# Performance work log

Measured on AMD Instinct MI355X. Metric: run time of the kernel, lower is better.

## Reference

```python
import jax, jax.numpy as jnp
import numpy as np

N = 100000   # graph is [N, N]
NNZ = 1600000
D = 32

def setup_inputs() -> dict:
    key = jax.random.key(0)
    k1, k2, k3 = jax.random.split(key, 3)
    indices = jax.random.randint(k1, (2, NNZ), 0, N, dtype=jnp.int64)
    values = jax.random.uniform(k2, (NNZ,), dtype=jnp.float32)
    x = jax.random.normal(k3, (N, D), dtype=jnp.float32)
    return {"indices": indices, "values": values, "x": x}

def reference(indices, values, x):
    # SimpleHypergraphConv with edge_dropout=0.0 (Dropout is identity):
    # out = sparse_coo(indices, values, [N, N]) @ x
    rows = indices[0]
    cols = indices[1]
    n_rows = x.shape[0]  # square graph
    # gather features of source nodes, scale by edge value, scatter-add to rows
    msgs = values[:, None] * x[cols]                      # [nnz, D]
    out = jax.ops.segment_sum(msgs, rows, num_segments=n_rows)  # [N, D]
    return out
```

## Files before the change

kernel.cpp:

```cpp
#include <hip/hip_runtime.h>


#define D 32
#define SBSHIFT 7
#define BSHIFT 5
#define RPB 32
#define NB128_MAX 1024
#define CHUNK 4096
#define EPT (CHUNK / 256)
#define NCH_MAX 512
#define MAXE 1024

typedef unsigned long long ull;

__global__ __launch_bounds__(256) void bin_sorted_kernel(
    const int* __restrict__ idx, const float* __restrict__ vals,
    ull* __restrict__ packed, unsigned short* __restrict__ desc,
    int nnz, int nb)
{
    __shared__ int cnt[NB128_MAX];
    __shared__ int off[NB128_MAX + 1];
    __shared__ int sm[256];

    int chunk = blockIdx.x;
    int base = chunk * CHUNK;
    int m = min(CHUNK, nnz - base);

    for (int i = threadIdx.x; i < nb; i += 256) cnt[i] = 0;
    __syncthreads();

    ull pv[EPT];
    int pb[EPT];
    #pragma unroll
    for (int j = 0; j < EPT; ++j) {
        int i = threadIdx.x + j * 256;
        pb[j] = -1;
        if (i < m) {
            int e = base + i;
            int r = idx[e];
            unsigned c = (unsigned)idx[nnz + e];
            unsigned vb = __float_as_uint(vals[e]);
            pv[j] = ((ull)vb << 32) | ((ull)c << SBSHIFT) | (unsigned)(r & 127);
            pb[j] = r >> SBSHIFT;
            atomicAdd(&cnt[pb[j]], 1);
        }
    }
    __syncthreads();

    {
        int b4 = threadIdx.x * 4;
        int v0 = (b4 + 0 < nb) ? cnt[b4 + 0] : 0;
        int v1 = (b4 + 1 < nb) ? cnt[b4 + 1] : 0;
        int v2 = (b4 + 2 < nb) ? cnt[b4 + 2] : 0;
        int v3 = (b4 + 3 < nb) ? cnt[b4 + 3] : 0;
        int tot = v0 + v1 + v2 + v3;
        sm[threadIdx.x] = tot;
        __syncthreads();
        for (int o = 1; o < 256; o <<= 1) {
            int t = sm[threadIdx.x];
            int u = (threadIdx.x >= o) ? sm[threadIdx.x - o] : 0;
            __syncthreads();
            sm[threadIdx.x] = t + u;
            __syncthreads();
        }
        int ex = sm[threadIdx.x] - tot;
        if (b4 + 0 < nb) off[b4 + 0] = ex;
        if (b4 + 1 < nb) off[b4 + 1] = ex + v0;
        if (b4 + 2 < nb) off[b4 + 2] = ex + v0 + v1;
        if (b4 + 3 < nb) off[b4 + 3] = ex + v0 + v1 + v2;
        if (threadIdx.x == 0) off[nb] = m;
    }
    __syncthreads();

    for (int i = threadIdx.x; i < nb; i += 256) cnt[i] = off[i];
    __syncthreads();

    #pragma unroll
    for (int j = 0; j < EPT; ++j) {
        if (pb[j] >= 0) {
            int pos = atomicAdd(&cnt[pb[j]], 1);
            packed[(size_t)base + pos] = pv[j];
        }
    }

    for (int i = threadIdx.x; i <= nb; i += 256)
        desc[(size_t)chunk * (nb + 1) + i] = (unsigned short)off[i];
}

__global__ __launch_bounds__(256) void spmm_seg_kernel(
    const unsigned short* __restrict__ desc,
    const ull* __restrict__ packed,
    const float* __restrict__ x, float* __restrict__ out,
    int N, int nb, int nchunk)
{
    __shared__ ull sp[MAXE];
    __shared__ int cnt[RPB];
    __shared__ int off[RPB];
    __shared__ int cur[RPB];
    __shared__ int segScan[NCH_MAX + 1];
    __shared__ unsigned short segStart[NCH_MAX];
    __shared__ int sm2[256];

    int wg = blockIdx.x;
    int j = wg >> 2;
    int mysub = wg & 3;
    int g = threadIdx.x >> 3;
    int q = threadIdx.x & 7;
    const float4* __restrict__ x4 = reinterpret_cast<const float4*>(x);

    {
        int t = threadIdx.x;
        int c0 = 2 * t, c1 = 2 * t + 1;
        int len0 = 0, len1 = 0;
        if (c0 < nchunk) {
            int a = desc[(size_t)c0 * (nb + 1) + j];
            int bnd = desc[(size_t)c0 * (nb + 1) + j + 1];
            segStart[c0] = (unsigned short)a;
            len0 = bnd - a;
        } else if (c0 < NCH_MAX) segStart[c0] = 0;
        if (c1 < nchunk) {
            int a = desc[(size_t)c1 * (nb + 1) + j];
            int bnd = desc[(size_t)c1 * (nb + 1) + j + 1];
            segStart[c1] = (unsigned short)a;
            len1 = bnd - a;
        } else if (c1 < NCH_MAX) segStart[c1] = 0;
        int tot = len0 + len1;
        sm2[t] = tot;
        __syncthreads();
        for (int o = 1; o < 256; o <<= 1) {
            int v = sm2[t];
            int u = (t >= o) ? sm2[t - o] : 0;
            __syncthreads();
            sm2[t] = v + u;
            __syncthreads();
        }
        int ex = sm2[t] - tot;
        segScan[c0] = ex;
        segScan[c1] = ex + len0;
        if (t == 255) segScan[NCH_MAX] = sm2[255];
        __syncthreads();
    }
    int total = segScan[NCH_MAX];

    float4 acc = make_float4(0.f, 0.f, 0.f, 0.f);

    for (int bb = 0; bb < total; bb += MAXE) {
        int m = min(MAXE, total - bb);

        if (threadIdx.x < RPB) cnt[threadIdx.x] = 0;
        __syncthreads();

        ull pv[MAXE / 256];
        bool have[MAXE / 256];
        #pragma unroll
        for (int jj = 0; jj < MAXE / 256; ++jj) {
            int i = threadIdx.x + jj * 256;
            have[jj] = false;
            if (i < m) {
                int gi = bb + i;
                int c = 0;
                #pragma unroll
                for (int st = 256; st >= 1; st >>= 1) {
                    int nc2 = c + st;
                    if (nc2 <= NCH_MAX - 1 && segScan[nc2] <= gi) c = nc2;
                }
                ull p = packed[(size_t)c * CHUNK + (int)segStart[c] + (gi - segScan[c])];
                if ((int)((p >> BSHIFT) & 3) == mysub) {
                    pv[jj] = p;
                    have[jj] = true;
                    atomicAdd(&cnt[(int)(p & (RPB - 1))], 1);
                }
            }
        }
        __syncthreads();

        if (threadIdx.x < RPB) {
            int v = cnt[threadIdx.x];
            int sum = v;
            #pragma unroll
            for (int d2 = 1; d2 < RPB; d2 <<= 1) {
                int u = __shfl_up(sum, d2, 64);
                if ((int)threadIdx.x >= d2) sum += u;
            }
            off[threadIdx.x] = sum - v;
            cur[threadIdx.x] = sum - v;
        }
        __syncthreads();

        #pragma unroll
        for (int jj = 0; jj < MAXE / 256; ++jj) {
            if (have[jj]) {
                int rl = (int)(pv[jj] & (RPB - 1));
                int pos = atomicAdd(&cur[rl], 1);
                sp[pos] = pv[jj];
            }
        }
        __syncthreads();

        int rs = off[g];
        int re = rs + cnt[g];
        int k = rs;
        for (; k + 3 < re; k += 4) {
            ull p0 = sp[k], p1 = sp[k + 1], p2 = sp[k + 2], p3 = sp[k + 3];
            int c0 = (int)((p0 >> SBSHIFT) & 0x1ffff);
            int c1 = (int)((p1 >> SBSHIFT) & 0x1ffff);
            int c2 = (int)((p2 >> SBSHIFT) & 0x1ffff);
            int c3 = (int)((p3 >> SBSHIFT) & 0x1ffff);
            float v0 = __uint_as_float((unsigned)(p0 >> 32));
            float v1 = __uint_as_float((unsigned)(p1 >> 32));
            float v2 = __uint_as_float((unsigned)(p2 >> 32));
            float v3 = __uint_as_float((unsigned)(p3 >> 32));
            float4 a0 = x4[(size_t)c0 * (D / 4) + q];
            float4 a1 = x4[(size_t)c1 * (D / 4) + q];
            float4 a2 = x4[(size_t)c2 * (D / 4) + q];
            float4 a3 = x4[(size_t)c3 * (D / 4) + q];
            acc.x += v0 * a0.x; acc.y += v0 * a0.y; acc.z += v0 * a0.z; acc.w += v0 * a0.w;
            acc.x += v1 * a1.x; acc.y += v1 * a1.y; acc.z += v1 * a1.z; acc.w += v1 * a1.w;
            acc.x += v2 * a2.x; acc.y += v2 * a2.y; acc.z += v2 * a2.z; acc.w += v2 * a2.w;
            acc.x += v3 * a3.x; acc.y += v3 * a3.y; acc.z += v3 * a3.z; acc.w += v3 * a3.w;
        }
        for (; k < re; ++k) {
            ull p = sp[k];
            int c = (int)((p >> SBSHIFT) & 0x1ffff);
            float v = __uint_as_float((unsigned)(p >> 32));
            float4 a = x4[(size_t)c * (D / 4) + q];
            acc.x += v * a.x; acc.y += v * a.y; acc.z += v * a.z; acc.w += v * a.w;
        }
        __syncthreads();
    }

    int row = (j << SBSHIFT) + (mysub << BSHIFT) + g;
    if (row < N)
        reinterpret_cast<float4*>(out)[(size_t)row * (D / 4) + q] = acc;
}

__global__ __launch_bounds__(256) void spmm_scatter_kernel(
    const int* __restrict__ idx, const float* __restrict__ vals,
    const float* __restrict__ x, float* __restrict__ out, int nnz)
{
    int t = blockIdx.x * blockDim.x + threadIdx.x;
    int e = t >> 3;
    int q = t & 7;
    if (e >= nnz) return;
    int r = idx[e];
    int c = idx[nnz + e];
    float v = vals[e];
    const float4 xv = reinterpret_cast<const float4*>(x)[(size_t)c * (D / 4) + q];
    float* o = out + (size_t)r * D + q * 4;
    atomicAdd(o + 0, v * xv.x);
    atomicAdd(o + 1, v * xv.y);
    atomicAdd(o + 2, v * xv.z);
    atomicAdd(o + 3, v * xv.w);
}

static inline size_t align256(size_t v) { return (v + 255) & ~(size_t)255; }

extern "C" void kernel_launch(void* const* d_in, const int* in_sizes, int n_in,
                              void* d_out, int out_size, void* d_ws, size_t ws_size,
                              hipStream_t stream)
{
    const int* idx   = (const int*)d_in[0];
    const float* val = (const float*)d_in[1];
    const float* x   = (const float*)d_in[2];
    float* out       = (float*)d_out;

    const int nnz   = in_sizes[1];
    const int N     = out_size / D;
    const int nb128 = (N + 127) >> SBSHIFT;
    const int nb32  = (N + 31) >> BSHIFT;
    const int nchunk = (nnz + CHUNK - 1) / CHUNK;

    size_t off_packed = 0;
    size_t off_desc   = align256(off_packed + (size_t)nnz * 8);
    size_t ws_needed  = off_desc + (size_t)nchunk * (nb128 + 1) * 2;

    if (ws_size < ws_needed || nb128 > NB128_MAX || nchunk > NCH_MAX || N > 131072) {
        hipMemsetAsync(d_out, 0, (size_t)out_size * sizeof(float), stream);
        const long long total = (long long)nnz * 8;
        spmm_scatter_kernel<<<(int)((total + 255) / 256), 256, 0, stream>>>(
            idx, val, x, out, nnz);
        return;
    }

    char* ws = (char*)d_ws;
    ull* packed = (ull*)(ws + off_packed);
    unsigned short* desc = (unsigned short*)(ws + off_desc);

    bin_sorted_kernel<<<nchunk, 256, 0, stream>>>(idx, val, packed, desc, nnz, nb128);
    spmm_seg_kernel<<<nb32, 256, 0, stream>>>(desc, packed, x, out, N, nb128, nchunk);
}
```

Before: 73.77 us.

## Process each 128-row bin with one 1024-thread block instead of four

The SpMM stage now uses one 1024-thread workgroup per 128-row super-bin, where before it used four 256-thread workgroups that each re-read the whole bin and filtered out three quarters of the entries. Each packed entry is now read once and local-sorted by its 7-bit row, with a shared-memory scan over 128 counts. This removes the redundant reading and filtering of packed data and the repeated descriptor scans. In exchange there are 4x fewer, larger blocks (about 782), scans that need more __syncthreads with 1024 threads, and a larger shared staging buffer.

```diff
diff --git a/kernel.cpp b/kernel.cpp
--- a/kernel.cpp
+++ b/kernel.cpp
@@ -3,13 +3,11 @@
 
 #define D 32
 #define SBSHIFT 7
-#define BSHIFT 5
-#define RPB 32
 #define NB128_MAX 1024
 #define CHUNK 4096
 #define EPT (CHUNK / 256)
 #define NCH_MAX 512
-#define MAXE 1024
+#define MAXB 2048
 
 typedef unsigned long long ull;
 
@@ -87,110 +85,98 @@
         desc[(size_t)chunk * (nb + 1) + i] = (unsigned short)off[i];
 }
 
-__global__ __launch_bounds__(256) void spmm_seg_kernel(
+__global__ __launch_bounds__(1024, 8) void spmm_sb_kernel(
     const unsigned short* __restrict__ desc,
     const ull* __restrict__ packed,
     const float* __restrict__ x, float* __restrict__ out,
     int N, int nb, int nchunk)
 {
-    __shared__ ull sp[MAXE];
-    __shared__ int cnt[RPB];
-    __shared__ int off[RPB];
-    __shared__ int cur[RPB];
+    __shared__ ull sp[MAXB];
+    __shared__ int cnt[128];
+    __shared__ int off[128];
+    __shared__ int cur[128];
     __shared__ int segScan[NCH_MAX + 1];
     __shared__ unsigned short segStart[NCH_MAX];
-    __shared__ int sm2[256];
-
-    int wg = blockIdx.x;
-    int j = wg >> 2;
-    int mysub = wg & 3;
-    int g = threadIdx.x >> 3;
-    int q = threadIdx.x & 7;
+    __shared__ int sm2[NCH_MAX];
+
+    int j = blockIdx.x;
+    int t = threadIdx.x;
+    int g = t >> 3;
+    int q = t & 7;
     const float4* __restrict__ x4 = reinterpret_cast<const float4*>(x);
 
-    {
-        int t = threadIdx.x;
-        int c0 = 2 * t, c1 = 2 * t + 1;
-        int len0 = 0, len1 = 0;
-        if (c0 < nchunk) {
-            int a = desc[(size_t)c0 * (nb + 1) + j];
-            int bnd = desc[(size_t)c0 * (nb + 1) + j + 1];
-            segStart[c0] = (unsigned short)a;
-            len0 = bnd - a;
-        } else if (c0 < NCH_MAX) segStart[c0] = 0;
-        if (c1 < nchunk) {
-            int a = desc[(size_t)c1 * (nb + 1) + j];
-            int bnd = desc[(size_t)c1 * (nb + 1) + j + 1];
-            segStart[c1] = (unsigned short)a;
-            len1 = bnd - a;
-        } else if (c1 < NCH_MAX) segStart[c1] = 0;
-        int tot = len0 + len1;
-        sm2[t] = tot;
-        __syncthreads();
-        for (int o = 1; o < 256; o <<= 1) {
-            int v = sm2[t];
-            int u = (t >= o) ? sm2[t - o] : 0;
-            __syncthreads();
-            sm2[t] = v + u;
-            __syncthreads();
-        }
-        int ex = sm2[t] - tot;
-        segScan[c0] = ex;
-        segScan[c1] = ex + len0;
-        if (t == 255) segScan[NCH_MAX] = sm2[255];
-        __syncthreads();
-    }
+    int len = 0;
+    if (t < nchunk) {
+        int a  = desc[(size_t)t * (nb + 1) + j];
+        int bd = desc[(size_t)t * (nb + 1) + j + 1];
+        segStart[t] = (unsigned short)a;
+        len = bd - a;
+    } else if (t < NCH_MAX) {
+        segStart[t] = 0;
+    }
+    if (t < NCH_MAX) sm2[t] = len;
+    __syncthreads();
+    for (int o = 1; o < NCH_MAX; o <<= 1) {
+        int v = 0;
+        if (t < NCH_MAX) { v = sm2[t]; if (t >= o) v += sm2[t - o]; }
+        __syncthreads();
+        if (t < NCH_MAX) sm2[t] = v;
+        __syncthreads();
+    }
+    if (t < NCH_MAX) segScan[t] = sm2[t] - len;
+    if (t == NCH_MAX - 1) segScan[NCH_MAX] = sm2[t];
+    __syncthreads();
     int total = segScan[NCH_MAX];
 
     float4 acc = make_float4(0.f, 0.f, 0.f, 0.f);
 
-    for (int bb = 0; bb < total; bb += MAXE) {
-        int m = min(MAXE, total - bb);
-
-        if (threadIdx.x < RPB) cnt[threadIdx.x] = 0;
-        __syncthreads();
-
-        ull pv[MAXE / 256];
-        bool have[MAXE / 256];
+    for (int bb = 0; bb < total; bb += MAXB) {
+        int m = min(MAXB, total - bb);
+
+        if (t < 128) cnt[t] = 0;
+        __syncthreads();
+
+        ull pv[MAXB / 1024];
+        bool have[MAXB / 1024];
         #pragma unroll
-        for (int jj = 0; jj < MAXE / 256; ++jj) {
-            int i = threadIdx.x + jj * 256;
-            have[jj] = false;
-            if (i < m) {
+        for (int jj = 0; jj < MAXB / 1024; ++jj) {
+            int i = t + jj * 1024;
+            have[jj] = (i < m);
+            if (have[jj]) {
                 int gi = bb + i;
                 int c = 0;
                 #pragma unroll
-                for (int st = 256; st >= 1; st >>= 1) {
-                    int nc2 = c + st;
-                    if (nc2 <= NCH_MAX - 1 && segScan[nc2] <= gi) c = nc2;
+                for (int st = NCH_MAX / 2; st >= 1; st >>= 1) {
+                    int nc = c + st;
+                    if (nc <= NCH_MAX - 1 && segScan[nc] <= gi) c = nc;
                 }
                 ull p = packed[(size_t)c * CHUNK + (int)segStart[c] + (gi - segScan[c])];
-                if ((int)((p >> BSHIFT) & 3) == mysub) {
-                    pv[jj] = p;
-                    have[jj] = true;
-                    atomicAdd(&cnt[(int)(p & (RPB - 1))], 1);
-                }
+                pv[jj] = p;
+                atomicAdd(&cnt[(int)(p & 127)], 1);
             }
         }
         __syncthreads();
 
-        if (threadIdx.x < RPB) {
-            int v = cnt[threadIdx.x];
-            int sum = v;
-            #pragma unroll
-            for (int d2 = 1; d2 < RPB; d2 <<= 1) {
-                int u = __shfl_up(sum, d2, 64);
-                if ((int)threadIdx.x >= d2) sum += u;
-            }
-            off[threadIdx.x] = sum - v;
-            cur[threadIdx.x] = sum - v;
+        if (t < 128) sm2[t] = cnt[t];
+        __syncthreads();
+        for (int o = 1; o < 128; o <<= 1) {
+            int v = 0;
+            if (t < 128) { v = sm2[t]; if (t >= o) v += sm2[t - o]; }
+            __syncthreads();
+            if (t < 128) sm2[t] = v;
+            __syncthreads();
+        }
+        if (t < 128) {
+            int ex = sm2[t] - cnt[t];
+            off[t] = ex;
+            cur[t] = ex;
         }
         __syncthreads();
 
         #pragma unroll
-        for (int jj = 0; jj < MAXE / 256; ++jj) {
+        for (int jj = 0; jj < MAXB / 1024; ++jj) {
             if (have[jj]) {
-                int rl = (int)(pv[jj] & (RPB - 1));
+                int rl = (int)(pv[jj] & 127);
                 int pos = atomicAdd(&cur[rl], 1);
                 sp[pos] = pv[jj];
             }
@@ -229,7 +215,7 @@
         __syncthreads();
     }
 
-    int row = (j << SBSHIFT) + (mysub << BSHIFT) + g;
+    int row = (j << SBSHIFT) + g;
     if (row < N)
         reinterpret_cast<float4*>(out)[(size_t)row * (D / 4) + q] = acc;
 }
@@ -267,7 +253,6 @@
     const int nnz   = in_sizes[1];
     const int N     = out_size / D;
     const int nb128 = (N + 127) >> SBSHIFT;
-    const int nb32  = (N + 31) >> BSHIFT;
     const int nchunk = (nnz + CHUNK - 1) / CHUNK;
 
     size_t off_packed = 0;
@@ -287,5 +272,5 @@
     unsigned short* desc = (unsigned short*)(ws + off_desc);
 
     bin_sorted_kernel<<<nchunk, 256, 0, stream>>>(idx, val, packed, desc, nnz, nb128);
-    spmm_seg_kernel<<<nb32, 256, 0, stream>>>(desc, packed, x, out, N, nb128, nchunk);
-}
+    spmm_sb_kernel<<<nb128, 1024, 0, stream>>>(desc, packed, x, out, N, nb128, nchunk);
+}
```

After: 63.86 us, median of 2. -13.4%, faster.
